# Kernel optimization log

Measured on AMD Instinct MI355X. Metric: run time of the kernel, lower is better.

Reference implementation:

```python
import jax, jax.numpy as jnp
import numpy as np


def setup_inputs() -> dict:
    key = jax.random.key(0)
    k1, k2 = jax.random.split(key)
    n_nodes, d_feat, n_edges = 100000, 48, 1600000
    x = jax.random.normal(k1, (n_nodes, d_feat), dtype=jnp.float32)
    edge_index = jax.random.randint(k2, (2, n_edges), 0, n_nodes, dtype=jnp.int64)
    return {"x": x, "edge_index": edge_index, "batch_size": 65536}


def reference(x, edge_index, batch_size):
    # adj = SparseTensor.from_edge_index(edge_index): adj[row, col] = 1 with
    # row = edge_index[0] (src), col = edge_index[1] (dst).
    # adj.t() @ x  ->  out[i] = sum over edges (src -> i) of x[src]
    src, dst = edge_index[0], edge_index[1]
    n_nodes = x.shape[0]
    # memory-bound gather + scatter-add (SpMM, sum aggregation)
    x_neighbors_sum = jax.ops.segment_sum(x[src], dst, num_segments=n_nodes)
    node_labels = jnp.concatenate(
        (x[:batch_size, :], x_neighbors_sum[:batch_size, :]), axis=-1
    )
    return node_labels
```

## Files before the change

kernel.cpp:

```cpp
#include <hip/hip_runtime.h>
#include <hip/hip_fp16.h>

#define DFEAT 48
#define OUTW  96
#define NBINB 512
#define BINTH 512
#define EPT   7
#define SORTCAP 3584
#define NBUCK2 512
#define RBITS 7
#define NROWS 128
#define RAWCAP 2560
#define CSRCAP 2560


static __device__ __forceinline__ unsigned short f2h(float f) {
    __half h = __float2half_rn(f);
    return *reinterpret_cast<unsigned short*>(&h);
}

static __device__ __forceinline__ int wave_iscan(int v, int lane) {
    #pragma unroll
    for (int d = 1; d < 64; d <<= 1) {
        int tv = __shfl_up(v, d, 64);
        if (lane >= d) v += tv;
    }
    return v;
}

__global__ __launch_bounds__(BINTH)
void bin_k(const int* __restrict__ ei, int n_edges, int batch, int chunk,
           const float4* __restrict__ x4, int nx4, uint2* __restrict__ xh4,
           unsigned short* __restrict__ starts, unsigned int* __restrict__ regions,
           float4* __restrict__ out4, int use_half) {
    __shared__ int cnt[NBUCK2];
    __shared__ int cur[NBUCK2];
    __shared__ int wsum[BINTH / 64];
    __shared__ int totS;
    __shared__ unsigned int sorted[SORTCAP];
    const int t = threadIdx.x;
    const int b = blockIdx.x;
    const int lane = t & 63, wid = t >> 6;

    if (use_half) {
        const int batch12 = batch * 12;
        for (int i = b * BINTH + t; i < nx4; i += NBINB * BINTH) {
            float4 v = x4[i];
            xh4[i] = make_uint2((unsigned)f2h(v.x) | ((unsigned)f2h(v.y) << 16),
                                (unsigned)f2h(v.z) | ((unsigned)f2h(v.w) << 16));
            if (i < batch12) {
                int row = i / 12, cg = i - row * 12;
                out4[(size_t)row * 24 + cg] = v;
            }
        }
    }

    const int beg = b * chunk;
    const int end = min(beg + chunk, n_edges);

    unsigned int pay[EPT];
    int bkt[EPT];
    #pragma unroll
    for (int i = 0; i < EPT; i++) {
        bkt[i] = -1;
        int e = beg + t + i * BINTH;
        if (e < end) {
            int dst = ei[n_edges + e];
            if (dst < batch) {
                int src = ei[e];
                bkt[i] = dst >> RBITS;
                pay[i] = ((unsigned)(dst & (NROWS - 1)) << 17) | (unsigned)src;
            }
        }
    }
    cnt[t] = 0;
    __syncthreads();
    #pragma unroll
    for (int i = 0; i < EPT; i++)
        if (bkt[i] >= 0) atomicAdd(&cnt[bkt[i]], 1);
    __syncthreads();
    int v = cnt[t];
    int iv = wave_iscan(v, lane);
    if (lane == 63) wsum[wid] = iv;
    __syncthreads();
    if (t < BINTH / 64) {
        int wv = wsum[t];
        int sv = wave_iscan(wv, t);
        wsum[t] = sv - wv;
        if (t == BINTH / 64 - 1) totS = sv;
    }
    __syncthreads();
    int excl = iv - v + wsum[wid];
    int tot = totS;
    cur[t] = excl;
    starts[t * NBINB + b] = (unsigned short)excl;
    if (t == 0) starts[NBUCK2 * NBINB + b] = (unsigned short)tot;
    __syncthreads();
    #pragma unroll
    for (int i = 0; i < EPT; i++)
        if (bkt[i] >= 0) {
            int pos = atomicAdd(&cur[bkt[i]], 1);
            sorted[pos] = pay[i];
        }
    __syncthreads();
    unsigned int* reg = regions + (size_t)b * chunk;
    for (int i = t; i < tot; i += BINTH) reg[i] = sorted[i];
}

__global__ __launch_bounds__(1024)
void reduce_k(const float* __restrict__ x, const uint4* __restrict__ xh4,
              const unsigned short* __restrict__ starts,
              const unsigned int* __restrict__ regions,
              float* __restrict__ out, int batch, int chunk, int use_half) {
    __shared__ unsigned int raw[RAWCAP];
    __shared__ int csr[CSRCAP];
    __shared__ int cnt[NROWS], off[NROWS + 1], cur[NROWS];
    __shared__ int rbase[NBINB], rs[NBINB], rl[NBINB];
    __shared__ int wsum[16];
    __shared__ int totS;
    const int t = threadIdx.x;
    const int kb = blockIdx.x;
    const int lane = t & 63, wid = t >> 6;

    int s0 = 0, len = 0;
    if (t < NBINB) {
        s0 = starts[kb * NBINB + t];
        int s1 = starts[(kb + 1) * NBINB + t];
        len = s1 - s0;
    }
    int iv = wave_iscan(len, lane);
    if (lane == 63 && wid < 8) wsum[wid] = iv;
    __syncthreads();
    if (t < 8) {
        int wv = wsum[t];
        int sv = wave_iscan(wv, t);
        wsum[t] = sv - wv;
        if (t == 7) totS = sv;
    }
    __syncthreads();
    if (t < NBINB) {
        rbase[t] = iv - len + wsum[wid];
        rs[t] = s0;
        rl[t] = len;
    }
    __syncthreads();
    const int T = min(totS, RAWCAP);
    {
        int r = t >> 1, h = t & 1;
        int L = rl[r], base = rbase[r];
        const unsigned int* reg = regions + (size_t)r * chunk + rs[r];
        if (L <= 8) {
            #pragma unroll
            for (int i = 0; i < 4; i++) {
                int idx = h + 2 * i;
                if (idx < L) {
                    int p = base + idx;
                    if (p < RAWCAP) raw[p] = reg[idx];
                }
            }
        } else {
            for (int idx = h; idx < L; idx += 2) {
                int p = base + idx;
                if (p < RAWCAP) raw[p] = reg[idx];
            }
        }
    }
    if (t < NROWS) cnt[t] = 0;
    __syncthreads();
    for (int i = t; i < T; i += 1024) atomicAdd(&cnt[raw[i] >> 17], 1);
    __syncthreads();
    int v2 = (t < NROWS) ? cnt[t] : 0;
    int iv2 = wave_iscan(v2, lane);
    if (lane == 63 && wid < 2) wsum[wid] = iv2;
    __syncthreads();
    if (t == 0) {
        int a = wsum[0];
        off[NROWS] = a + wsum[1];
        wsum[1] = a;
        wsum[0] = 0;
    }
    __syncthreads();
    if (t < NROWS) {
        int excl = iv2 - v2 + wsum[wid];
        off[t] = excl;
        cur[t] = excl;
    }
    __syncthreads();
    for (int i = t; i < T; i += 1024) {
        unsigned int p = raw[i];
        int pos = atomicAdd(&cur[p >> 17], 1);
        if (pos < CSRCAP) csr[pos] = (int)(p & 0x1FFFFu) * 6;
    }
    __syncthreads();

    if (use_half) {
        const int g   = lane / 6;
        const int cg  = lane - g * 6;
        const bool act = lane < 48;
        const bool isA = g < 4;
        const int gg  = isA ? g : g - 4;
        float4* out4 = (float4*)out;
        #pragma unroll
        for (int rr = 0; rr < 4; rr++) {
            const int ra = wid + 16 * rr;
            const int rb = ra + 64;
            const int rowA = kb * NROWS + ra;
            const int rowB = kb * NROWS + rb;
            const bool okA = rowA < batch, okB = rowB < batch;
            int e0a = 0, e1a = 0, e0b = 0, e1b = 0;
            if (okA) { e0a = off[ra]; e1a = min(off[ra + 1], CSRCAP); }
            if (okB) { e0b = off[rb]; e1b = min(off[rb + 1], CSRCAP); }
            const int e0 = isA ? e0a : e0b;
            const int e1 = isA ? e1a : e1b;
            float a0=0.f,a1=0.f,a2=0.f,a3=0.f,a4=0.f,a5=0.f,a6=0.f,a7=0.f;
            const int n = max(e1a - e0a, e1b - e0b);
            for (int k = 0; k < n; k += 16) {
                const int i1 = e0 + k + gg;
                const int i2 = i1 + 4;
                const int i3 = i1 + 8;
                const int i4 = i1 + 12;
                const bool v1 = act && i1 < e1;
                const bool v2 = act && i2 < e1;
                const bool v3 = act && i3 < e1;
                const bool v4 = act && i4 < e1;
                const int c1 = v1 ? csr[min(i1, CSRCAP - 1)] : 0;
                const int c2 = v2 ? csr[min(i2, CSRCAP - 1)] : 0;
                const int c3 = v3 ? csr[min(i3, CSRCAP - 1)] : 0;
                const int c4 = v4 ? csr[min(i4, CSRCAP - 1)] : 0;
                const uint4 p1 = xh4[(size_t)c1 + cg];
                const uint4 p2 = xh4[(size_t)c2 + cg];
                const uint4 p3 = xh4[(size_t)c3 + cg];
                const uint4 p4 = xh4[(size_t)c4 + cg];
                if (v1) {
                    float2 f0 = __half22float2(*(const __half2*)&p1.x);
                    float2 f1 = __half22float2(*(const __half2*)&p1.y);
                    float2 f2 = __half22float2(*(const __half2*)&p1.z);
                    float2 f3 = __half22float2(*(const __half2*)&p1.w);
                    a0 += f0.x; a1 += f0.y; a2 += f1.x; a3 += f1.y;
                    a4 += f2.x; a5 += f2.y; a6 += f3.x; a7 += f3.y;
                }
                if (v2) {
                    float2 f0 = __half22float2(*(const __half2*)&p2.x);
                    float2 f1 = __half22float2(*(const __half2*)&p2.y);
                    float2 f2 = __half22float2(*(const __half2*)&p2.z);
                    float2 f3 = __half22float2(*(const __half2*)&p2.w);
                    a0 += f0.x; a1 += f0.y; a2 += f1.x; a3 += f1.y;
                    a4 += f2.x; a5 += f2.y; a6 += f3.x; a7 += f3.y;
                }
                if (v3) {
                    float2 f0 = __half22float2(*(const __half2*)&p3.x);
                    float2 f1 = __half22float2(*(const __half2*)&p3.y);
                    float2 f2 = __half22float2(*(const __half2*)&p3.z);
                    float2 f3 = __half22float2(*(const __half2*)&p3.w);
                    a0 += f0.x; a1 += f0.y; a2 += f1.x; a3 += f1.y;
                    a4 += f2.x; a5 += f2.y; a6 += f3.x; a7 += f3.y;
                }
                if (v4) {
                    float2 f0 = __half22float2(*(const __half2*)&p4.x);
                    float2 f1 = __half22float2(*(const __half2*)&p4.y);
                    float2 f2 = __half22float2(*(const __half2*)&p4.z);
                    float2 f3 = __half22float2(*(const __half2*)&p4.w);
                    a0 += f0.x; a1 += f0.y; a2 += f1.x; a3 += f1.y;
                    a4 += f2.x; a5 += f2.y; a6 += f3.x; a7 += f3.y;
                }
            }
            float b0,b1,b2,b3,b4,b5,b6,b7;
            b0=__shfl(a0,lane+12); b1=__shfl(a1,lane+12);
            b2=__shfl(a2,lane+12); b3=__shfl(a3,lane+12);
            b4=__shfl(a4,lane+12); b5=__shfl(a5,lane+12);
            b6=__shfl(a6,lane+12); b7=__shfl(a7,lane+12);
            a0+=b0; a1+=b1; a2+=b2; a3+=b3; a4+=b4; a5+=b5; a6+=b6; a7+=b7;
            b0=__shfl(a0,lane+6); b1=__shfl(a1,lane+6);
            b2=__shfl(a2,lane+6); b3=__shfl(a3,lane+6);
            b4=__shfl(a4,lane+6); b5=__shfl(a5,lane+6);
            b6=__shfl(a6,lane+6); b7=__shfl(a7,lane+6);
            a0+=b0; a1+=b1; a2+=b2; a3+=b3; a4+=b4; a5+=b5; a6+=b6; a7+=b7;
            if (okA && lane < 6) {
                out4[(size_t)rowA * 24 + 12 + cg * 2]     = make_float4(a0,a1,a2,a3);
                out4[(size_t)rowA * 24 + 12 + cg * 2 + 1] = make_float4(a4,a5,a6,a7);
            }
            if (okB && lane >= 24 && lane < 30) {
                out4[(size_t)rowB * 24 + 12 + cg * 2]     = make_float4(a0,a1,a2,a3);
                out4[(size_t)rowB * 24 + 12 + cg * 2 + 1] = make_float4(a4,a5,a6,a7);
            }
        }
    } else {
        if (lane < DFEAT) {
            for (int r = wid; r < NROWS; r += 16) {
                int row = kb * NROWS + r;
                if (row >= batch) break;
                int e0 = off[r], e1 = min(off[r + 1], CSRCAP);
                float acc = 0.f;
                for (int e = e0; e < e1; ++e)
                    acc += x[(size_t)csr[e] * 8 + lane];
                out[(size_t)row * OUTW + lane]         = x[(size_t)row * DFEAT + lane];
                out[(size_t)row * OUTW + DFEAT + lane] = acc;
            }
        }
    }
}


#define D4   12
#define ROW4 24

__global__ void init_out_kernel(const float4* __restrict__ x4,
                                float4* __restrict__ out4, int batch) {
    int idx = blockIdx.x * blockDim.x + threadIdx.x;
    int total = batch * ROW4;
    if (idx >= total) return;
    int row = idx / ROW4;
    int c   = idx - row * ROW4;
    float4 v;
    if (c < D4) v = x4[row * D4 + c];
    else        v = make_float4(0.f, 0.f, 0.f, 0.f);
    out4[idx] = v;
}

__global__ void scatter_edges_kernel(const float4* __restrict__ x4,
                                     const int* __restrict__ ei,
                                     float* __restrict__ out,
                                     int n_edges, int batch) {
    int tid = blockIdx.x * blockDim.x + threadIdx.x;
    int e = tid / D4;
    int q = tid - e * D4;
    if (e >= n_edges) return;
    int dst = ei[n_edges + e];
    if (dst >= batch) return;
    int src = ei[e];
    float4 v = x4[src * D4 + q];
    float* p = out + (size_t)dst * OUTW + DFEAT + q * 4;
    atomicAdd(p + 0, v.x);
    atomicAdd(p + 1, v.y);
    atomicAdd(p + 2, v.z);
    atomicAdd(p + 3, v.w);
}


extern "C" void kernel_launch(void* const* d_in, const int* in_sizes, int n_in,
                              void* d_out, int out_size, void* d_ws, size_t ws_size,
                              hipStream_t stream) {
    const float* x  = (const float*)d_in[0];
    const int*   ei = (const int*)d_in[1];
    float* out = (float*)d_out;

    const int n_edges = in_sizes[1] / 2;
    const int batch   = out_size / OUTW;
    const int n_nodes = in_sizes[0] / DFEAT;
    const int chunk   = (n_edges + NBINB - 1) / NBINB;
    const int nbuck   = (batch + NROWS - 1) / NROWS;
    const int nx4     = n_nodes * DFEAT / 4;

    size_t xh_bytes = ((size_t)n_nodes * DFEAT * sizeof(unsigned short) + 15) & ~(size_t)15;
    size_t starts_bytes = (size_t)(NBUCK2 + 1) * NBINB * sizeof(unsigned short);
    size_t reg_bytes = (size_t)NBINB * chunk * sizeof(unsigned int);
    size_t need_h = xh_bytes + starts_bytes + reg_bytes;
    size_t need_f = starts_bytes + reg_bytes;

    bool base_ok = chunk <= SORTCAP && chunk <= BINTH * EPT && chunk < 65536 &&
                   n_nodes <= (1 << 17) && batch <= NBUCK2 * NROWS &&
                   (n_nodes * DFEAT) % 4 == 0 && nbuck >= 1 && nbuck <= NBUCK2 &&
                   batch % NROWS == 0;

    if (base_ok && ws_size >= need_h) {
        unsigned short* xh = (unsigned short*)d_ws;
        unsigned short* starts = (unsigned short*)((char*)d_ws + xh_bytes);
        unsigned int* regions = (unsigned int*)((char*)d_ws + xh_bytes + starts_bytes);
        bin_k<<<NBINB, BINTH, 0, stream>>>(ei, n_edges, batch, chunk,
                                           (const float4*)x, nx4, (uint2*)xh,
                                           starts, regions, (float4*)out, 1);
        reduce_k<<<nbuck, 1024, 0, stream>>>(x, (const uint4*)xh, starts, regions,
                                             out, batch, chunk, 1);
    } else if (base_ok && ws_size >= need_f) {
        unsigned short* starts = (unsigned short*)d_ws;
        unsigned int* regions = (unsigned int*)((char*)d_ws + starts_bytes);
        bin_k<<<NBINB, BINTH, 0, stream>>>(ei, n_edges, batch, chunk,
                                           (const float4*)x, nx4, (uint2*)0,
                                           starts, regions, (float4*)out, 0);
        reduce_k<<<nbuck, 1024, 0, stream>>>(x, (const uint4*)0, starts, regions,
                                             out, batch, chunk, 0);
    } else {
        {
            int total = batch * ROW4;
            int grid = (total + 255) / 256;
            init_out_kernel<<<grid, 256, 0, stream>>>((const float4*)x,
                                                      (float4*)out, batch);
        }
        {
            long long total = (long long)n_edges * D4;
            long long grid = (total + 255) / 256;
            scatter_edges_kernel<<<(int)grid, 256, 0, stream>>>(
                (const float4*)x, ei, out, n_edges, batch);
        }
    }
}
```

Measured before the change: 119.1 us.

## Replace per-block CSR build with shared-memory atomic accumulation per row

Drops the in-block counting sort (count, scan, scatter into a CSR array) and instead has each edge directly atomically add its gathered neighbor features into a shared-memory accumulator tile of 128 rows by 49 floats. Edges are processed in flat order, so load balance no longer depends on per-row degree. Afterward the tile is written out with float4 stores. This removes several barriers and the scan, at the cost of many LDS float atomics with possible contention, and the summation order becomes nondeterministic.

```diff
diff --git a/kernel.cpp b/kernel.cpp
--- a/kernel.cpp
+++ b/kernel.cpp
@@ -11,7 +11,7 @@
 #define RBITS 7
 #define NROWS 128
 #define RAWCAP 2560
-#define CSRCAP 2560
+#define ACCW  49
 
 
 static __device__ __forceinline__ unsigned short f2h(float f) {
@@ -113,8 +113,7 @@
               const unsigned int* __restrict__ regions,
               float* __restrict__ out, int batch, int chunk, int use_half) {
     __shared__ unsigned int raw[RAWCAP];
-    __shared__ int csr[CSRCAP];
-    __shared__ int cnt[NROWS], off[NROWS + 1], cur[NROWS];
+    __shared__ float acc[NROWS][ACCW];
     __shared__ int rbase[NBINB], rs[NBINB], rl[NBINB];
     __shared__ int wsum[16];
     __shared__ int totS;
@@ -142,6 +141,10 @@
         rbase[t] = iv - len + wsum[wid];
         rs[t] = s0;
         rl[t] = len;
+    }
+    {
+        float* af = &acc[0][0];
+        for (int i = t; i < NROWS * ACCW; i += 1024) af[i] = 0.f;
     }
     __syncthreads();
     const int T = min(totS, RAWCAP);
@@ -165,136 +168,116 @@
             }
         }
     }
-    if (t < NROWS) cnt[t] = 0;
-    __syncthreads();
-    for (int i = t; i < T; i += 1024) atomicAdd(&cnt[raw[i] >> 17], 1);
-    __syncthreads();
-    int v2 = (t < NROWS) ? cnt[t] : 0;
-    int iv2 = wave_iscan(v2, lane);
-    if (lane == 63 && wid < 2) wsum[wid] = iv2;
-    __syncthreads();
-    if (t == 0) {
-        int a = wsum[0];
-        off[NROWS] = a + wsum[1];
-        wsum[1] = a;
-        wsum[0] = 0;
-    }
-    __syncthreads();
-    if (t < NROWS) {
-        int excl = iv2 - v2 + wsum[wid];
-        off[t] = excl;
-        cur[t] = excl;
-    }
-    __syncthreads();
-    for (int i = t; i < T; i += 1024) {
-        unsigned int p = raw[i];
-        int pos = atomicAdd(&cur[p >> 17], 1);
-        if (pos < CSRCAP) csr[pos] = (int)(p & 0x1FFFFu) * 6;
-    }
     __syncthreads();
 
     if (use_half) {
-        const int g   = lane / 6;
-        const int cg  = lane - g * 6;
-        const bool act = lane < 48;
-        const bool isA = g < 4;
-        const int gg  = isA ? g : g - 4;
+        const int slot = lane / 6;
+        const int cg   = lane - slot * 6;
+        const bool act = lane < 60;
+        for (int e0 = wid * 10; e0 < T; e0 += 640) {
+            const int e1 = e0 + slot;
+            const int e2 = e1 + 160;
+            const int e3 = e1 + 320;
+            const int e4 = e1 + 480;
+            const bool v1 = act && e1 < T;
+            const bool v2 = act && e2 < T;
+            const bool v3 = act && e3 < T;
+            const bool v4 = act && e4 < T;
+            const unsigned int w1 = raw[min(e1, T - 1)];
+            const unsigned int w2 = raw[min(e2, T - 1)];
+            const unsigned int w3 = raw[min(e3, T - 1)];
+            const unsigned int w4 = raw[min(e4, T - 1)];
+            const int s1 = v1 ? (int)(w1 & 0x1FFFFu) * 6 : 0;
+            const int s2 = v2 ? (int)(w2 & 0x1FFFFu) * 6 : 0;
+            const int s3 = v3 ? (int)(w3 & 0x1FFFFu) * 6 : 0;
+            const int s4 = v4 ? (int)(w4 & 0x1FFFFu) * 6 : 0;
+            const uint4 p1 = xh4[(size_t)s1 + cg];
+            const uint4 p2 = xh4[(size_t)s2 + cg];
+            const uint4 p3 = xh4[(size_t)s3 + cg];
+            const uint4 p4 = xh4[(size_t)s4 + cg];
+            if (v1) {
+                float2 f0 = __half22float2(*(const __half2*)&p1.x);
+                float2 f1 = __half22float2(*(const __half2*)&p1.y);
+                float2 f2 = __half22float2(*(const __half2*)&p1.z);
+                float2 f3 = __half22float2(*(const __half2*)&p1.w);
+                float* a = &acc[w1 >> 17][cg * 8];
+                atomicAdd(a + 0, f0.x); atomicAdd(a + 1, f0.y);
+                atomicAdd(a + 2, f1.x); atomicAdd(a + 3, f1.y);
+                atomicAdd(a + 4, f2.x); atomicAdd(a + 5, f2.y);
+                atomicAdd(a + 6, f3.x); atomicAdd(a + 7, f3.y);
+            }
+            if (v2) {
+                float2 f0 = __half22float2(*(const __half2*)&p2.x);
+                float2 f1 = __half22float2(*(const __half2*)&p2.y);
+                float2 f2 = __half22float2(*(const __half2*)&p2.z);
+                float2 f3 = __half22float2(*(const __half2*)&p2.w);
+                float* a = &acc[w2 >> 17][cg * 8];
+                atomicAdd(a + 0, f0.x); atomicAdd(a + 1, f0.y);
+                atomicAdd(a + 2, f1.x); atomicAdd(a + 3, f1.y);
+                atomicAdd(a + 4, f2.x); atomicAdd(a + 5, f2.y);
+                atomicAdd(a + 6, f3.x); atomicAdd(a + 7, f3.y);
+            }
+            if (v3) {
+                float2 f0 = __half22float2(*(const __half2*)&p3.x);
+                float2 f1 = __half22float2(*(const __half2*)&p3.y);
+                float2 f2 = __half22float2(*(const __half2*)&p3.z);
+                float2 f3 = __half22float2(*(const __half2*)&p3.w);
+                float* a = &acc[w3 >> 17][cg * 8];
+                atomicAdd(a + 0, f0.x); atomicAdd(a + 1, f0.y);
+                atomicAdd(a + 2, f1.x); atomicAdd(a + 3, f1.y);
+                atomicAdd(a + 4, f2.x); atomicAdd(a + 5, f2.y);
+                atomicAdd(a + 6, f3.x); atomicAdd(a + 7, f3.y);
+            }
+            if (v4) {
+                float2 f0 = __half22float2(*(const __half2*)&p4.x);
+                float2 f1 = __half22float2(*(const __half2*)&p4.y);
+                float2 f2 = __half22float2(*(const __half2*)&p4.z);
+                float2 f3 = __half22float2(*(const __half2*)&p4.w);
+                float* a = &acc[w4 >> 17][cg * 8];
+                atomicAdd(a + 0, f0.x); atomicAdd(a + 1, f0.y);
+                atomicAdd(a + 2, f1.x); atomicAdd(a + 3, f1.y);
+                atomicAdd(a + 4, f2.x); atomicAdd(a + 5, f2.y);
+                atomicAdd(a + 6, f3.x); atomicAdd(a + 7, f3.y);
+            }
+        }
+        __syncthreads();
         float4* out4 = (float4*)out;
-        #pragma unroll
-        for (int rr = 0; rr < 4; rr++) {
-            const int ra = wid + 16 * rr;
-            const int rb = ra + 64;
-            const int rowA = kb * NROWS + ra;
-            const int rowB = kb * NROWS + rb;
-            const bool okA = rowA < batch, okB = rowB < batch;
-            int e0a = 0, e1a = 0, e0b = 0, e1b = 0;
-            if (okA) { e0a = off[ra]; e1a = min(off[ra + 1], CSRCAP); }
-            if (okB) { e0b = off[rb]; e1b = min(off[rb + 1], CSRCAP); }
-            const int e0 = isA ? e0a : e0b;
-            const int e1 = isA ? e1a : e1b;
-            float a0=0.f,a1=0.f,a2=0.f,a3=0.f,a4=0.f,a5=0.f,a6=0.f,a7=0.f;
-            const int n = max(e1a - e0a, e1b - e0b);
-            for (int k = 0; k < n; k += 16) {
-                const int i1 = e0 + k + gg;
-                const int i2 = i1 + 4;
-                const int i3 = i1 + 8;
-                const int i4 = i1 + 12;
-                const bool v1 = act && i1 < e1;
-                const bool v2 = act && i2 < e1;
-                const bool v3 = act && i3 < e1;
-                const bool v4 = act && i4 < e1;
-                const int c1 = v1 ? csr[min(i1, CSRCAP - 1)] : 0;
-                const int c2 = v2 ? csr[min(i2, CSRCAP - 1)] : 0;
-                const int c3 = v3 ? csr[min(i3, CSRCAP - 1)] : 0;
-                const int c4 = v4 ? csr[min(i4, CSRCAP - 1)] : 0;
-                const uint4 p1 = xh4[(size_t)c1 + cg];
-                const uint4 p2 = xh4[(size_t)c2 + cg];
-                const uint4 p3 = xh4[(size_t)c3 + cg];
-                const uint4 p4 = xh4[(size_t)c4 + cg];
-                if (v1) {
-                    float2 f0 = __half22float2(*(const __half2*)&p1.x);
-                    float2 f1 = __half22float2(*(const __half2*)&p1.y);
-                    float2 f2 = __half22float2(*(const __half2*)&p1.z);
-                    float2 f3 = __half22float2(*(const __half2*)&p1.w);
-                    a0 += f0.x; a1 += f0.y; a2 += f1.x; a3 += f1.y;
-                    a4 += f2.x; a5 += f2.y; a6 += f3.x; a7 += f3.y;
-                }
-                if (v2) {
-                    float2 f0 = __half22float2(*(const __half2*)&p2.x);
-                    float2 f1 = __half22float2(*(const __half2*)&p2.y);
-                    float2 f2 = __half22float2(*(const __half2*)&p2.z);
-                    float2 f3 = __half22float2(*(const __half2*)&p2.w);
-                    a0 += f0.x; a1 += f0.y; a2 += f1.x; a3 += f1.y;
-                    a4 += f2.x; a5 += f2.y; a6 += f3.x; a7 += f3.y;
-                }
-                if (v3) {
-                    float2 f0 = __half22float2(*(const __half2*)&p3.x);
-                    float2 f1 = __half22float2(*(const __half2*)&p3.y);
-                    float2 f2 = __half22float2(*(const __half2*)&p3.z);
-                    float2 f3 = __half22float2(*(const __half2*)&p3.w);
-                    a0 += f0.x; a1 += f0.y; a2 += f1.x; a3 += f1.y;
-                    a4 += f2.x; a5 += f2.y; a6 += f3.x; a7 += f3.y;
-                }
-                if (v4) {
-                    float2 f0 = __half22float2(*(const __half2*)&p4.x);
-                    float2 f1 = __half22float2(*(const __half2*)&p4.y);
-                    float2 f2 = __half22float2(*(const __half2*)&p4.z);
-                    float2 f3 = __half22float2(*(const __half2*)&p4.w);
-                    a0 += f0.x; a1 += f0.y; a2 += f1.x; a3 += f1.y;
-                    a4 += f2.x; a5 += f2.y; a6 += f3.x; a7 += f3.y;
-                }
-            }
-            float b0,b1,b2,b3,b4,b5,b6,b7;
-            b0=__shfl(a0,lane+12); b1=__shfl(a1,lane+12);
-            b2=__shfl(a2,lane+12); b3=__shfl(a3,lane+12);
-            b4=__shfl(a4,lane+12); b5=__shfl(a5,lane+12);
-            b6=__shfl(a6,lane+12); b7=__shfl(a7,lane+12);
-            a0+=b0; a1+=b1; a2+=b2; a3+=b3; a4+=b4; a5+=b5; a6+=b6; a7+=b7;
-            b0=__shfl(a0,lane+6); b1=__shfl(a1,lane+6);
-            b2=__shfl(a2,lane+6); b3=__shfl(a3,lane+6);
-            b4=__shfl(a4,lane+6); b5=__shfl(a5,lane+6);
-            b6=__shfl(a6,lane+6); b7=__shfl(a7,lane+6);
-            a0+=b0; a1+=b1; a2+=b2; a3+=b3; a4+=b4; a5+=b5; a6+=b6; a7+=b7;
-            if (okA && lane < 6) {
-                out4[(size_t)rowA * 24 + 12 + cg * 2]     = make_float4(a0,a1,a2,a3);
-                out4[(size_t)rowA * 24 + 12 + cg * 2 + 1] = make_float4(a4,a5,a6,a7);
-            }
-            if (okB && lane >= 24 && lane < 30) {
-                out4[(size_t)rowB * 24 + 12 + cg * 2]     = make_float4(a0,a1,a2,a3);
-                out4[(size_t)rowB * 24 + 12 + cg * 2 + 1] = make_float4(a4,a5,a6,a7);
+        for (int i = t; i < NROWS * 12; i += 1024) {
+            int r = i / 12, cg2 = i - r * 12;
+            int row = kb * NROWS + r;
+            if (row < batch) {
+                const float* a = &acc[r][cg2 * 4];
+                out4[(size_t)row * 24 + 12 + cg2] =
+                    make_float4(a[0], a[1], a[2], a[3]);
             }
         }
     } else {
-        if (lane < DFEAT) {
-            for (int r = wid; r < NROWS; r += 16) {
-                int row = kb * NROWS + r;
-                if (row >= batch) break;
-                int e0 = off[r], e1 = min(off[r + 1], CSRCAP);
-                float acc = 0.f;
-                for (int e = e0; e < e1; ++e)
-                    acc += x[(size_t)csr[e] * 8 + lane];
-                out[(size_t)row * OUTW + lane]         = x[(size_t)row * DFEAT + lane];
-                out[(size_t)row * OUTW + DFEAT + lane] = acc;
+        const float4* x4r = (const float4*)x;
+        const int slot = lane / 12;
+        const int cg   = lane - slot * 12;
+        const bool act = lane < 60;
+        for (int e0 = wid * 5; e0 < T; e0 += 80) {
+            int e = e0 + slot;
+            if (act && e < T) {
+                unsigned int w = raw[e];
+                int row = w >> 17;
+                int s = (int)(w & 0x1FFFFu) * 12;
+                float4 p = x4r[(size_t)s + cg];
+                float* a = &acc[row][cg * 4];
+                atomicAdd(a + 0, p.x); atomicAdd(a + 1, p.y);
+                atomicAdd(a + 2, p.z); atomicAdd(a + 3, p.w);
+            }
+        }
+        __syncthreads();
+        float4* out4 = (float4*)out;
+        for (int i = t; i < NROWS * 12; i += 1024) {
+            int r = i / 12, cg2 = i - r * 12;
+            int row = kb * NROWS + r;
+            if (row < batch) {
+                out4[(size_t)row * 24 + cg2] = x4r[(size_t)row * 12 + cg2];
+                const float* a = &acc[r][cg2 * 4];
+                out4[(size_t)row * 24 + 12 + cg2] =
+                    make_float4(a[0], a[1], a[2], a[3]);
             }
         }
     }
```

Measured after the change: 360.7 us. +202.9%, slower.
